# Performance work log

Hardware: AMD Instinct MI355X
Metric: run time of the kernel (lower is better)

## Reference

```python
import jax, jax.numpy as jnp
import numpy as np

N = 2048
E = 512
H = 8
DH = E // H
L = 2
MAX_DIST = 10
LOCAL_DIST = 2
NUM_COLORS = 16
NEG_INF = -1e9


def _layer_norm(x, scale, bias, eps=1e-5):
    mu = jnp.mean(x, axis=-1, keepdims=True)
    var = jnp.mean(jnp.square(x - mu), axis=-1, keepdims=True)
    return (x - mu) * jax.lax.rsqrt(var + eps) * scale + bias


def setup_inputs() -> dict:
    key = jax.random.key(0)
    ks = jax.random.split(key, 12)
    s = 0.05  # weight init scale for numerical sanity
    return {
        "D": jax.random.randint(ks[0], (N, N), 0, MAX_DIST + 2, dtype=jnp.int32),
        "x": jax.random.normal(ks[1], (1, N, E), dtype=jnp.float32),
        "dist_emb": jax.random.normal(ks[2], (MAX_DIST + 2, 8), dtype=jnp.float32) * s,
        "dist_proj_w": jax.random.normal(ks[3], (1, 8), dtype=jnp.float32) * s,
        "dist_proj_b": jnp.zeros((1,), jnp.float32),
        "ln1_scale": jnp.ones((L, E), jnp.float32),
        "ln1_bias": jnp.zeros((L, E), jnp.float32),
        "in_proj_w": jax.random.normal(ks[4], (L, 3 * E, E), dtype=jnp.float32) * s,
        "in_proj_b": jnp.zeros((L, 3 * E), jnp.float32),
        "out_w": jax.random.normal(ks[5], (L, E, E), dtype=jnp.float32) * s,
        "out_b": jnp.zeros((L, E), jnp.float32),
        "ln2_scale": jnp.ones((L, E), jnp.float32),
        "ln2_bias": jnp.zeros((L, E), jnp.float32),
        "ff1_w": jax.random.normal(ks[6], (L, 2 * E, E), dtype=jnp.float32) * s,
        "ff1_b": jnp.zeros((L, 2 * E), jnp.float32),
        "ff2_w": jax.random.normal(ks[7], (L, E, 2 * E), dtype=jnp.float32) * s,
        "ff2_b": jnp.zeros((L, E), jnp.float32),
        "color_w": jax.random.normal(ks[8], (NUM_COLORS, E), dtype=jnp.float32) * s,
        "color_b": jnp.zeros((NUM_COLORS,), jnp.float32),
    }


def reference(D, x, dist_emb, dist_proj_w, dist_proj_b,
              ln1_scale, ln1_bias, in_proj_w, in_proj_b, out_w, out_b,
              ln2_scale, ln2_bias, ff1_w, ff1_b, ff2_w, ff2_b,
              color_w, color_b):
    # Distance encoder: clamp -> embed -> project to scalar bias per (i, j)
    d_clamped = jnp.clip(D, 0, MAX_DIST + 1)                        # [N, N]
    emb = dist_emb[d_clamped]                                       # [N, N, 8]
    bias = jnp.einsum('nme,e->nm', emb, dist_proj_w[0]) + dist_proj_b[0]
    # Graph-local sparsity: real bias within local_dist, -inf elsewhere
    attn_mask = jnp.where(D <= LOCAL_DIST, bias, NEG_INF)           # [N, N]

    scale = 1.0 / jnp.sqrt(jnp.asarray(DH, x.dtype))
    for l in range(L):
        # --- pre-norm multihead self-attention ---
        xn = _layer_norm(x, ln1_scale[l], ln1_bias[l])              # [1, N, E]
        qkv = jnp.einsum('bne,fe->bnf', xn, in_proj_w[l]) + in_proj_b[l]
        q, k, v = jnp.split(qkv, 3, axis=-1)                        # each [1, N, E]
        q = q.reshape(1, N, H, DH)
        k = k.reshape(1, N, H, DH)
        v = v.reshape(1, N, H, DH)
        scores = jnp.einsum('bnhd,bmhd->bhnm', q, k) * scale        # [1, H, N, N]
        scores = scores + attn_mask[None, None, :, :]
        probs = jax.nn.softmax(scores, axis=-1)
        attn = jnp.einsum('bhnm,bmhd->bnhd', probs, v).reshape(1, N, E)
        attn = jnp.einsum('bne,fe->bnf', attn, out_w[l]) + out_b[l]
        x = x + attn                                                # dropout = identity (eval)
        # --- pre-norm feed-forward ---
        xf = _layer_norm(x, ln2_scale[l], ln2_bias[l])
        h = jax.nn.relu(jnp.einsum('bne,fe->bnf', xf, ff1_w[l]) + ff1_b[l])
        ff = jnp.einsum('bnf,ef->bne', h, ff2_w[l]) + ff2_b[l]
        x = x + ff

    logits = jnp.einsum('bne,ce->bnc', x, color_w) + color_b        # [1, N, C]
    return jax.nn.softmax(logits, axis=-1)[0]                       # [N, C]
```

## Files before the change

### kernel.cpp

```cpp
#include <hip/hip_runtime.h>
#include <cstddef>
#include <cstdint>

#define NN 2048
#define EE 512
#define HH 8
#define QKVF 1536
#define NSEG 4

typedef __attribute__((ext_vector_type(4))) float f32x4;
typedef __attribute__((ext_vector_type(8))) short s16x8;
typedef __attribute__((ext_vector_type(4))) short s16x4;

static __device__ __forceinline__ unsigned short f2bf(float x) {
  union { float f; unsigned int u; } c; c.f = x;
  unsigned int r = (c.u + 0x7FFFu + ((c.u >> 16) & 1u)) >> 16;
  return (unsigned short)r;
}
static __device__ __forceinline__ float bf2f(unsigned short b) {
  union { unsigned int u; float f; } c; c.u = ((unsigned int)b) << 16;
  return c.f;
}

#define GLL16(gp, lp) __builtin_amdgcn_global_load_lds( \
    (const __attribute__((address_space(1))) void*)(gp), \
    (__attribute__((address_space(3))) void*)(lp), 16, 0, 0)

__global__ __launch_bounds__(256) void cvt_all(
    const float* __restrict__ s0, const float* __restrict__ s1,
    const float* __restrict__ s2, const float* __restrict__ s3,
    unsigned short* __restrict__ d0, unsigned short* __restrict__ d1,
    unsigned short* __restrict__ d2, unsigned short* __restrict__ d3,
    int n0, int n1, int n2, int n3) {
  int j = blockIdx.x * 256 + threadIdx.x;
  const float* s; unsigned short* d;
  if (j < n0) { s = s0; d = d0; }
  else {
    j -= n0;
    if (j < n1) { s = s1; d = d1; }
    else {
      j -= n1;
      if (j < n2) { s = s2; d = d2; }
      else { j -= n2; if (j >= n3) return; s = s3; d = d3; }
    }
  }
  float4 v = ((const float4*)s)[j];
  s16x4 o;
  o[0] = (short)f2bf(v.x); o[1] = (short)f2bf(v.y);
  o[2] = (short)f2bf(v.z); o[3] = (short)f2bf(v.w);
  ((s16x4*)d)[j] = o;
}

__global__ __launch_bounds__(256) void mask_pack(const int* __restrict__ D,
    unsigned int* __restrict__ codes) {
  int id = blockIdx.x * 256 + threadIdx.x;
  int row = id >> 9;
  int u = id & 511;
  int ch = u >> 4, col = u & 15;
  int base = ch * 64 + col;
  unsigned int pk = 0;
#pragma unroll
  for (int i = 0; i < 4; i++) {
    int d = D[(size_t)row * NN + base + 16 * i];
    unsigned int c = (d <= 2) ? (unsigned int)d : 3u;
    pk |= c << (8 * i);
  }
  codes[id] = pk;
}

__global__ __launch_bounds__(256) void ln_kernel(const float* __restrict__ x,
    const float* __restrict__ scale, const float* __restrict__ bias,
    unsigned short* __restrict__ out) {
  int row = blockIdx.x;
  int t = threadIdx.x;
  const float* xr = x + (size_t)row * EE;
  float a = xr[t], b = xr[t + 256];
  float s = a + b, q = a * a + b * b;
#pragma unroll
  for (int m = 1; m < 64; m <<= 1) {
    s += __shfl_xor(s, m);
    q += __shfl_xor(q, m);
  }
  __shared__ float ps[4], pq[4];
  int w = t >> 6;
  if ((t & 63) == 0) { ps[w] = s; pq[w] = q; }
  __syncthreads();
  s = ps[0] + ps[1] + ps[2] + ps[3];
  q = pq[0] + pq[1] + pq[2] + pq[3];
  float mu = s * (1.f / EE);
  float var = q * (1.f / EE) - mu * mu;
  float r = rsqrtf(var + 1e-5f);
  unsigned short* orow = out + (size_t)row * EE;
  orow[t] = f2bf((a - mu) * r * scale[t] + bias[t]);
  orow[t + 256] = f2bf((b - mu) * r * scale[t + 256] + bias[t + 256]);
}

template <int RELU, int RES, int OBF>
__global__ __launch_bounds__(256) void gemm_bf(
    const unsigned short* __restrict__ A, const unsigned short* __restrict__ B,
    const float* __restrict__ bias, const float* __restrict__ R,
    void* __restrict__ Cout, int M, int F, int K) {
  __shared__ __attribute__((aligned(16))) unsigned short Al[2][64 * 64];
  __shared__ __attribute__((aligned(16))) unsigned short Bl[2][64 * 64];
  const int t = threadIdx.x;
  const int w = t >> 6, l = t & 63;
  const int fr = l & 15, fs = l >> 4;
  const int bm = blockIdx.y * 64, bf = blockIdx.x * 64;
  const int srow = l >> 3, slot = l & 7;
  const int nk = K >> 6;

  f32x4 acc[4];
  f32x4 zero = {0.f, 0.f, 0.f, 0.f};
#pragma unroll
  for (int j = 0; j < 4; j++) acc[j] = zero;

  auto stage = [&](int kt, int bsel) {
    int k0 = kt * 64;
#pragma unroll
    for (int rnd = 0; rnd < 2; rnd++) {
      int rowblk = w * 2 + rnd;
      int row = rowblk * 8 + srow;
      int koff = (slot * 8) ^ ((row & 7) * 8);
      GLL16(A + (size_t)(bm + row) * K + k0 + koff, &Al[bsel][rowblk * 512]);
      GLL16(B + (size_t)(bf + row) * K + k0 + koff, &Bl[bsel][rowblk * 512]);
    }
  };

  stage(0, 0);
  __syncthreads();
  for (int kt = 0; kt < nk; kt++) {
    const int cur = kt & 1;
    if (kt + 1 < nk) stage(kt + 1, cur ^ 1);
    s16x8 af[2], bg[4][2];
    const int arow = w * 16 + fr;
#pragma unroll
    for (int ks = 0; ks < 2; ks++)
      af[ks] = *(const s16x8*)&Al[cur][arow * 64 + ((ks * 32 + fs * 8) ^ ((arow & 7) * 8))];
#pragma unroll
    for (int ni = 0; ni < 4; ni++)
#pragma unroll
      for (int ks = 0; ks < 2; ks++) {
        int row = 16 * ni + fr;
        bg[ni][ks] = *(const s16x8*)&Bl[cur][row * 64 + ((ks * 32 + fs * 8) ^ ((row & 7) * 8))];
      }
#pragma unroll
    for (int ni = 0; ni < 4; ni++)
#pragma unroll
      for (int ks = 0; ks < 2; ks++)
        acc[ni] = __builtin_amdgcn_mfma_f32_16x16x32_bf16(af[ks], bg[ni][ks], acc[ni], 0, 0, 0);
    __syncthreads();
  }

#pragma unroll
  for (int ni = 0; ni < 4; ni++) {
    int gcol = bf + 16 * ni + fr;
    float bb = bias[gcol];
#pragma unroll
    for (int r = 0; r < 4; r++) {
      int grow = bm + w * 16 + fs * 4 + r;
      float v = acc[ni][r] + bb;
      if (RELU) v = fmaxf(v, 0.f);
      if (RES) v += R[(size_t)grow * F + gcol];
      if (OBF) ((unsigned short*)Cout)[(size_t)grow * F + gcol] = f2bf(v);
      else ((float*)Cout)[(size_t)grow * F + gcol] = v;
    }
  }
}

__global__ __launch_bounds__(256) void attn_mfma(
    const unsigned short* __restrict__ qkv, const unsigned int* __restrict__ codes,
    const float* __restrict__ demb, const float* __restrict__ dpw,
    const float* __restrict__ dpb, float* __restrict__ po, float* __restrict__ lpart) {
  __shared__ __attribute__((aligned(16))) unsigned short Kl[64 * 64];
  __shared__ __attribute__((aligned(16))) unsigned short Vt[64 * 64];
  __shared__ __attribute__((aligned(16))) unsigned short Pl[4][16 * 64];
  const int t = threadIdx.x;
  const int w = t >> 6, l = t & 63;
  const int fr = l & 15, fs = l >> 4;
  const int h = blockIdx.y;
  const int seg = blockIdx.z;
  const int qrow0 = blockIdx.x * 64 + w * 16;
  const int kvbase = seg * (NN / NSEG);
  const float C2 = 0.18033688011112042f;

  float w0, w1, w2;
  {
    float s0 = 0.f, s1 = 0.f, s2 = 0.f;
#pragma unroll
    for (int e = 0; e < 8; e++) {
      float pw = dpw[e];
      s0 += demb[e] * pw; s1 += demb[8 + e] * pw; s2 += demb[16 + e] * pw;
    }
    float b = dpb[0];
    w0 = __expf(s0 + b); w1 = __expf(s1 + b); w2 = __expf(s2 + b);
  }

  s16x8 qf[2];
#pragma unroll
  for (int ks = 0; ks < 2; ks++)
    qf[ks] = *(const s16x8*)&qkv[(size_t)(qrow0 + fr) * QKVF + h * 64 + ks * 32 + fs * 8];

  f32x4 o[4];
  float lacc[4];
  f32x4 zero = {0.f, 0.f, 0.f, 0.f};
#pragma unroll
  for (int i = 0; i < 4; i++) { o[i] = zero; lacc[i] = 0.f; }

  const int krow = t >> 2, kc = (t & 3) * 16;
  const int vkv = (t & 15) * 4, vd = (t >> 4) * 4;
  const unsigned short* kbase = qkv + EE + h * 64;
  const unsigned short* vbase = qkv + 2 * EE + h * 64;
  s16x8 kreg[2];
  s16x4 vreg[4];
#pragma unroll
  for (int i = 0; i < 2; i++)
    kreg[i] = *(const s16x8*)&kbase[(size_t)(kvbase + krow) * QKVF + kc + i * 8];
#pragma unroll
  for (int i = 0; i < 4; i++)
    vreg[i] = *(const s16x4*)&vbase[(size_t)(kvbase + vkv + i) * QKVF + vd];

  for (int ch = 0; ch < NN / NSEG / 64; ch++) {
    __syncthreads();
#pragma unroll
    for (int i = 0; i < 2; i++)
      *(s16x8*)&Kl[krow * 64 + ((kc + i * 8) ^ ((krow & 7) * 8))] = kreg[i];
#pragma unroll
    for (int dj = 0; dj < 4; dj++) {
      int d = vd + dj;
      s16x4 pk;
      pk[0] = vreg[0][dj]; pk[1] = vreg[1][dj]; pk[2] = vreg[2][dj]; pk[3] = vreg[3][dj];
      *(s16x4*)&Vt[d * 64 + (vkv ^ ((d & 7) * 8))] = pk;
    }
    __syncthreads();
    if (ch + 1 < NN / NSEG / 64) {
      int kv0 = kvbase + (ch + 1) * 64;
#pragma unroll
      for (int i = 0; i < 2; i++)
        kreg[i] = *(const s16x8*)&kbase[(size_t)(kv0 + krow) * QKVF + kc + i * 8];
#pragma unroll
      for (int i = 0; i < 4; i++)
        vreg[i] = *(const s16x4*)&vbase[(size_t)(kv0 + vkv + i) * QKVF + vd];
    }
    int gc = kvbase / 64 + ch;
    unsigned int cd[4];
#pragma unroll
    for (int r = 0; r < 4; r++)
      cd[r] = codes[(size_t)(qrow0 + fs * 4 + r) * (NN / 4) + gc * 16 + fr];

    f32x4 s[4];
#pragma unroll
    for (int ni = 0; ni < 4; ni++) s[ni] = zero;
    __builtin_amdgcn_s_setprio(1);
#pragma unroll
    for (int ni = 0; ni < 4; ni++) {
      int row = 16 * ni + fr;
#pragma unroll
      for (int ks = 0; ks < 2; ks++) {
        s16x8 kf = *(const s16x8*)&Kl[row * 64 + ((ks * 32 + fs * 8) ^ ((row & 7) * 8))];
        s[ni] = __builtin_amdgcn_mfma_f32_16x16x32_bf16(qf[ks], kf, s[ni], 0, 0, 0);
      }
    }
    __builtin_amdgcn_s_setprio(0);
#pragma unroll
    for (int r = 0; r < 4; r++) {
      int prow = fs * 4 + r;
      float psum = 0.f;
#pragma unroll
      for (int ni = 0; ni < 4; ni++) {
        unsigned int code = (cd[r] >> (8 * ni)) & 255u;
        float wsel = code == 0u ? w0 : (code == 1u ? w1 : (code == 2u ? w2 : 0.f));
        float p = exp2f(s[ni][r] * C2) * wsel;
        unsigned short pb = f2bf(p);
        psum += bf2f(pb);
        Pl[w][prow * 64 + ((16 * ni + fr) ^ ((prow & 7) * 8))] = pb;
      }
      lacc[r] += psum;
    }
    __builtin_amdgcn_s_setprio(1);
#pragma unroll
    for (int ks = 0; ks < 2; ks++) {
      s16x8 pa = *(const s16x8*)&Pl[w][fr * 64 + ((ks * 32 + fs * 8) ^ ((fr & 7) * 8))];
#pragma unroll
      for (int dn = 0; dn < 4; dn++) {
        int row = 16 * dn + fr;
        s16x8 vf = *(const s16x8*)&Vt[row * 64 + ((ks * 32 + fs * 8) ^ ((row & 7) * 8))];
        o[dn] = __builtin_amdgcn_mfma_f32_16x16x32_bf16(pa, vf, o[dn], 0, 0, 0);
      }
    }
    __builtin_amdgcn_s_setprio(0);
  }
#pragma unroll
  for (int r = 0; r < 4; r++) {
#pragma unroll
    for (int m = 1; m < 16; m <<= 1) lacc[r] += __shfl_xor(lacc[r], m);
  }
#pragma unroll
  for (int r = 0; r < 4; r++) {
    int row = qrow0 + fs * 4 + r;
#pragma unroll
    for (int dn = 0; dn < 4; dn++)
      po[((size_t)seg * NN + row) * EE + h * 64 + 16 * dn + fr] = o[dn][r];
    if (fr == 0) lpart[((size_t)seg * NN + row) * 8 + h] = lacc[r];
  }
}

__global__ __launch_bounds__(256) void attn_combine(const float* __restrict__ po,
    const float* __restrict__ lpart, unsigned short* __restrict__ attnb) {
  int id = blockIdx.x * 256 + threadIdx.x;
  int row = id >> 7;
  int col = (id & 127) * 4;
  int h = col >> 6;
  float4 o = {0.f, 0.f, 0.f, 0.f};
  float lsum = 0.f;
#pragma unroll
  for (int s = 0; s < NSEG; s++) {
    float4 p4 = *(const float4*)&po[((size_t)s * NN + row) * EE + col];
    o.x += p4.x; o.y += p4.y; o.z += p4.z; o.w += p4.w;
    lsum += lpart[((size_t)s * NN + row) * 8 + h];
  }
  float inv = 1.f / lsum;
  s16x4 ob;
  ob[0] = (short)f2bf(o.x * inv); ob[1] = (short)f2bf(o.y * inv);
  ob[2] = (short)f2bf(o.z * inv); ob[3] = (short)f2bf(o.w * inv);
  *(s16x4*)&attnb[(size_t)row * EE + col] = ob;
}

__global__ __launch_bounds__(256) void logits_kernel(const float* __restrict__ x,
    const float* __restrict__ cw, const float* __restrict__ cb,
    float* __restrict__ out) {
  int t = threadIdx.x;
  int wv = t >> 6, lane = t & 63;
  int row = blockIdx.x * 4 + wv;
  const float* xr = x + (size_t)row * EE;
  int c = lane >> 2, p = lane & 3;
  const float* w = cw + c * EE;
  float s = 0.f;
  for (int e = p * 128; e < p * 128 + 128; e++) s += xr[e] * w[e];
  s += __shfl_xor(s, 1);
  s += __shfl_xor(s, 2);
  __shared__ float lg[4][16];
  if (p == 0) lg[wv][c] = s + cb[c];
  __syncthreads();
  if (lane < 16) {
    float mx = -INFINITY;
#pragma unroll
    for (int k = 0; k < 16; k++) mx = fmaxf(mx, lg[wv][k]);
    float sum = 0.f;
#pragma unroll
    for (int k = 0; k < 16; k++) sum += __expf(lg[wv][k] - mx);
    out[(size_t)row * 16 + lane] = __expf(lg[wv][lane] - mx) / sum;
  }
}

extern "C" void kernel_launch(void* const* d_in, const int* in_sizes, int n_in,
                              void* d_out, int out_size, void* d_ws, size_t ws_size,
                              hipStream_t stream) {
  const int* D = (const int*)d_in[0];
  const float* x = (const float*)d_in[1];
  const float* demb = (const float*)d_in[2];
  const float* dpw = (const float*)d_in[3];
  const float* dpb = (const float*)d_in[4];
  const float* ln1s = (const float*)d_in[5];
  const float* ln1b = (const float*)d_in[6];
  const float* ipw = (const float*)d_in[7];
  const float* ipb = (const float*)d_in[8];
  const float* ow = (const float*)d_in[9];
  const float* ob = (const float*)d_in[10];
  const float* ln2s = (const float*)d_in[11];
  const float* ln2b = (const float*)d_in[12];
  const float* f1w = (const float*)d_in[13];
  const float* f1b = (const float*)d_in[14];
  const float* f2w = (const float*)d_in[15];
  const float* f2b = (const float*)d_in[16];
  const float* cw = (const float*)d_in[17];
  const float* cb = (const float*)d_in[18];

  char* base = (char*)d_ws;
  unsigned int* codes = (unsigned int*)base;
  float* xbuf = (float*)(base + (4u << 20));
  unsigned short* qkv = (unsigned short*)(base + (8u << 20));
  unsigned short* xn = (unsigned short*)(base + (14u << 20));
  unsigned short* attnb = (unsigned short*)(base + (16u << 20));
  unsigned short* hbuf = (unsigned short*)(base + (18u << 20));
  unsigned short* ipw_bf = (unsigned short*)(base + (22u << 20));
  unsigned short* ow_bf = (unsigned short*)(base + (25u << 20));
  unsigned short* f1w_bf = (unsigned short*)(base + (26u << 20));
  unsigned short* f2w_bf = (unsigned short*)(base + (28u << 20));
  float* po = (float*)(base + (31u << 20));
  float* lpart = (float*)(base + (47u << 20));

  cvt_all<<<4096, 256, 0, stream>>>(ipw, ow, f1w, f2w,
      ipw_bf, ow_bf, f1w_bf, f2w_bf, 393216, 131072, 262144, 262144);
  mask_pack<<<4096, 256, 0, stream>>>(D, codes);

  for (int l = 0; l < 2; l++) {
    const float* xin = (l == 0) ? x : xbuf;
    ln_kernel<<<NN, 256, 0, stream>>>(xin, ln1s + l * EE, ln1b + l * EE, xn);
    gemm_bf<0, 0, 1><<<dim3(24, 32), 256, 0, stream>>>(
        xn, ipw_bf + (size_t)l * 786432, ipb + l * 1536, nullptr, qkv, NN, 1536, 512);
    attn_mfma<<<dim3(32, HH, NSEG), 256, 0, stream>>>(qkv, codes, demb, dpw, dpb, po, lpart);
    attn_combine<<<1024, 256, 0, stream>>>(po, lpart, attnb);
    gemm_bf<0, 1, 0><<<dim3(8, 32), 256, 0, stream>>>(
        attnb, ow_bf + (size_t)l * 262144, ob + l * EE, xin, xbuf, NN, 512, 512);
    ln_kernel<<<NN, 256, 0, stream>>>(xbuf, ln2s + l * EE, ln2b + l * EE, xn);
    gemm_bf<1, 0, 1><<<dim3(16, 32), 256, 0, stream>>>(
        xn, f1w_bf + (size_t)l * 524288, f1b + l * 1024, nullptr, hbuf, NN, 1024, 512);
    gemm_bf<0, 1, 0><<<dim3(8, 32), 256, 0, stream>>>(
        hbuf, f2w_bf + (size_t)l * 524288, f2b + l * EE, xbuf, xbuf, NN, 512, 1024);
  }
  logits_kernel<<<NN / 4, 256, 0, stream>>>(xbuf, cw, cb, (float*)d_out);
}
```

Before: 316.0 us.

## Precompute per-pair mask weights, fold row-sum into MFMA, double KV split

Merges the weight conversion and mask packing into one prep kernel that stores the exponentiated distance weights as fp32 per (row, key) pair, so the attention loop no longer decodes codes. The softmax row sum is now produced by an extra MFMA against a row of ones in the V tile instead of scalar accumulation plus shuffles. Probabilities are truncated to bf16 rather than rounded. The key/value split count doubles from 4 to 8 to raise parallelism. In exchange, the mask array is four times larger (16MB instead of 4MB) and the partial-output buffers and combine pass also double in size.

```diff
diff --git a/kernel.cpp b/kernel.cpp
--- a/kernel.cpp
+++ b/kernel.cpp
@@ -6,7 +6,7 @@
 #define EE 512
 #define HH 8
 #define QKVF 1536
-#define NSEG 4
+#define NSEG 8
 
 typedef __attribute__((ext_vector_type(4))) float f32x4;
 typedef __attribute__((ext_vector_type(8))) short s16x8;
@@ -17,55 +17,59 @@
   unsigned int r = (c.u + 0x7FFFu + ((c.u >> 16) & 1u)) >> 16;
   return (unsigned short)r;
 }
-static __device__ __forceinline__ float bf2f(unsigned short b) {
-  union { unsigned int u; float f; } c; c.u = ((unsigned int)b) << 16;
-  return c.f;
-}
 
 #define GLL16(gp, lp) __builtin_amdgcn_global_load_lds( \
     (const __attribute__((address_space(1))) void*)(gp), \
     (__attribute__((address_space(3))) void*)(lp), 16, 0, 0)
 
-__global__ __launch_bounds__(256) void cvt_all(
+__global__ __launch_bounds__(256) void prep(
     const float* __restrict__ s0, const float* __restrict__ s1,
     const float* __restrict__ s2, const float* __restrict__ s3,
     unsigned short* __restrict__ d0, unsigned short* __restrict__ d1,
     unsigned short* __restrict__ d2, unsigned short* __restrict__ d3,
-    int n0, int n1, int n2, int n3) {
-  int j = blockIdx.x * 256 + threadIdx.x;
-  const float* s; unsigned short* d;
-  if (j < n0) { s = s0; d = d0; }
-  else {
-    j -= n0;
-    if (j < n1) { s = s1; d = d1; }
+    const int* __restrict__ D, const float* __restrict__ demb,
+    const float* __restrict__ dpw, const float* __restrict__ dpb,
+    float* __restrict__ wpk4) {
+  int b = blockIdx.x;
+  if (b < 4096) {
+    int j = b * 256 + threadIdx.x;
+    const float* s; unsigned short* d;
+    if (j < 393216) { s = s0; d = d0; }
     else {
-      j -= n1;
-      if (j < n2) { s = s2; d = d2; }
-      else { j -= n2; if (j >= n3) return; s = s3; d = d3; }
-    }
-  }
-  float4 v = ((const float4*)s)[j];
-  s16x4 o;
-  o[0] = (short)f2bf(v.x); o[1] = (short)f2bf(v.y);
-  o[2] = (short)f2bf(v.z); o[3] = (short)f2bf(v.w);
-  ((s16x4*)d)[j] = o;
-}
-
-__global__ __launch_bounds__(256) void mask_pack(const int* __restrict__ D,
-    unsigned int* __restrict__ codes) {
-  int id = blockIdx.x * 256 + threadIdx.x;
-  int row = id >> 9;
-  int u = id & 511;
-  int ch = u >> 4, col = u & 15;
-  int base = ch * 64 + col;
-  unsigned int pk = 0;
-#pragma unroll
-  for (int i = 0; i < 4; i++) {
-    int d = D[(size_t)row * NN + base + 16 * i];
-    unsigned int c = (d <= 2) ? (unsigned int)d : 3u;
-    pk |= c << (8 * i);
-  }
-  codes[id] = pk;
+      j -= 393216;
+      if (j < 131072) { s = s1; d = d1; }
+      else {
+        j -= 131072;
+        if (j < 262144) { s = s2; d = d2; }
+        else { j -= 262144; s = s3; d = d3; }
+      }
+    }
+    float4 v = ((const float4*)s)[j];
+    s16x4 o;
+    o[0] = (short)f2bf(v.x); o[1] = (short)f2bf(v.y);
+    o[2] = (short)f2bf(v.z); o[3] = (short)f2bf(v.w);
+    ((s16x4*)d)[j] = o;
+  } else {
+    int e = (b - 4096) * 256 + threadIdx.x;
+    float ws0 = 0.f, ws1 = 0.f, ws2 = 0.f;
+#pragma unroll
+    for (int k = 0; k < 8; k++) {
+      float pw = dpw[k];
+      ws0 += demb[k] * pw; ws1 += demb[8 + k] * pw; ws2 += demb[16 + k] * pw;
+    }
+    float bb = dpb[0];
+    float w0 = __expf(ws0 + bb), w1 = __expf(ws1 + bb), w2 = __expf(ws2 + bb);
+    int row = e >> 9;
+    int u = e & 511;
+    int base = (u >> 4) * 64 + (u & 15);
+    f32x4 wv;
+#pragma unroll
+    for (int i = 0; i < 4; i++) {
+      int d = D[(size_t)row * NN + base + 16 * i];
+      wv[i] = (d == 0) ? w0 : (d == 1) ? w1 : (d == 2) ? w2 : 0.f;
+    }
+    ((f32x4*)wpk4)[e] = wv;
+  }
 }
 
 __global__ __launch_bounds__(256) void ln_kernel(const float* __restrict__ x,
@@ -168,11 +172,10 @@
 }
 
 __global__ __launch_bounds__(256) void attn_mfma(
-    const unsigned short* __restrict__ qkv, const unsigned int* __restrict__ codes,
-    const float* __restrict__ demb, const float* __restrict__ dpw,
-    const float* __restrict__ dpb, float* __restrict__ po, float* __restrict__ lpart) {
+    const unsigned short* __restrict__ qkv, const float* __restrict__ wpk4,
+    float* __restrict__ po, float* __restrict__ lpart) {
   __shared__ __attribute__((aligned(16))) unsigned short Kl[64 * 64];
-  __shared__ __attribute__((aligned(16))) unsigned short Vt[64 * 64];
+  __shared__ __attribute__((aligned(16))) unsigned short Vt[66 * 64];
   __shared__ __attribute__((aligned(16))) unsigned short Pl[4][16 * 64];
   const int t = threadIdx.x;
   const int w = t >> 6, l = t & 63;
@@ -183,28 +186,18 @@
   const int kvbase = seg * (NN / NSEG);
   const float C2 = 0.18033688011112042f;
 
-  float w0, w1, w2;
-  {
-    float s0 = 0.f, s1 = 0.f, s2 = 0.f;
-#pragma unroll
-    for (int e = 0; e < 8; e++) {
-      float pw = dpw[e];
-      s0 += demb[e] * pw; s1 += demb[8 + e] * pw; s2 += demb[16 + e] * pw;
-    }
-    float b = dpb[0];
-    w0 = __expf(s0 + b); w1 = __expf(s1 + b); w2 = __expf(s2 + b);
-  }
+  if (t < 64) Vt[64 * 64 + t] = 0x3F80;
 
   s16x8 qf[2];
 #pragma unroll
   for (int ks = 0; ks < 2; ks++)
     qf[ks] = *(const s16x8*)&qkv[(size_t)(qrow0 + fr) * QKVF + h * 64 + ks * 32 + fs * 8];
 
-  f32x4 o[4];
-  float lacc[4];
+  f32x4 o[4], o4;
   f32x4 zero = {0.f, 0.f, 0.f, 0.f};
 #pragma unroll
-  for (int i = 0; i < 4; i++) { o[i] = zero; lacc[i] = 0.f; }
+  for (int i = 0; i < 4; i++) o[i] = zero;
+  o4 = zero;
 
   const int krow = t >> 2, kc = (t & 3) * 16;
   const int vkv = (t & 15) * 4, vd = (t >> 4) * 4;
@@ -242,10 +235,6 @@
         vreg[i] = *(const s16x4*)&vbase[(size_t)(kv0 + vkv + i) * QKVF + vd];
     }
     int gc = kvbase / 64 + ch;
-    unsigned int cd[4];
-#pragma unroll
-    for (int r = 0; r < 4; r++)
-      cd[r] = codes[(size_t)(qrow0 + fs * 4 + r) * (NN / 4) + gc * 16 + fr];
 
     f32x4 s[4];
 #pragma unroll
@@ -264,17 +253,14 @@
 #pragma unroll
     for (int r = 0; r < 4; r++) {
       int prow = fs * 4 + r;
-      float psum = 0.f;
+      f32x4 wv = *(const f32x4*)&wpk4[((size_t)(qrow0 + prow) * 512 + gc * 16 + fr) * 4];
 #pragma unroll
       for (int ni = 0; ni < 4; ni++) {
-        unsigned int code = (cd[r] >> (8 * ni)) & 255u;
-        float wsel = code == 0u ? w0 : (code == 1u ? w1 : (code == 2u ? w2 : 0.f));
-        float p = exp2f(s[ni][r] * C2) * wsel;
-        unsigned short pb = f2bf(p);
-        psum += bf2f(pb);
-        Pl[w][prow * 64 + ((16 * ni + fr) ^ ((prow & 7) * 8))] = pb;
-      }
-      lacc[r] += psum;
+        union { float f; unsigned int u; } c;
+        c.f = exp2f(s[ni][r] * C2) * wv[ni];
+        Pl[w][prow * 64 + ((16 * ni + fr) ^ ((prow & 7) * 8))] =
+            (unsigned short)(c.u >> 16);
+      }
     }
     __builtin_amdgcn_s_setprio(1);
 #pragma unroll
@@ -286,13 +272,10 @@
         s16x8 vf = *(const s16x8*)&Vt[row * 64 + ((ks * 32 + fs * 8) ^ ((row & 7) * 8))];
         o[dn] = __builtin_amdgcn_mfma_f32_16x16x32_bf16(pa, vf, o[dn], 0, 0, 0);
       }
+      s16x8 vf4 = *(const s16x8*)&Vt[(64 + fr) * 64 + ((ks * 32 + fs * 8) ^ ((fr & 7) * 8))];
+      o4 = __builtin_amdgcn_mfma_f32_16x16x32_bf16(pa, vf4, o4, 0, 0, 0);
     }
     __builtin_amdgcn_s_setprio(0);
-  }
-#pragma unroll
-  for (int r = 0; r < 4; r++) {
-#pragma unroll
-    for (int m = 1; m < 16; m <<= 1) lacc[r] += __shfl_xor(lacc[r], m);
   }
 #pragma unroll
   for (int r = 0; r < 4; r++) {
@@ -300,7 +283,7 @@
 #pragma unroll
     for (int dn = 0; dn < 4; dn++)
       po[((size_t)seg * NN + row) * EE + h * 64 + 16 * dn + fr] = o[dn][r];
-    if (fr == 0) lpart[((size_t)seg * NN + row) * 8 + h] = lacc[r];
+    if (fr == 0) lpart[((size_t)seg * NN + row) * 8 + h] = o4[r];
   }
 }
 
@@ -376,29 +359,28 @@
   const float* cb = (const float*)d_in[18];
 
   char* base = (char*)d_ws;
-  unsigned int* codes = (unsigned int*)base;
-  float* xbuf = (float*)(base + (4u << 20));
-  unsigned short* qkv = (unsigned short*)(base + (8u << 20));
-  unsigned short* xn = (unsigned short*)(base + (14u << 20));
-  unsigned short* attnb = (unsigned short*)(base + (16u << 20));
-  unsigned short* hbuf = (unsigned short*)(base + (18u << 20));
-  unsigned short* ipw_bf = (unsigned short*)(base + (22u << 20));
-  unsigned short* ow_bf = (unsigned short*)(base + (25u << 20));
-  unsigned short* f1w_bf = (unsigned short*)(base + (26u << 20));
-  unsigned short* f2w_bf = (unsigned short*)(base + (28u << 20));
-  float* po = (float*)(base + (31u << 20));
-  float* lpart = (float*)(base + (47u << 20));
-
-  cvt_all<<<4096, 256, 0, stream>>>(ipw, ow, f1w, f2w,
-      ipw_bf, ow_bf, f1w_bf, f2w_bf, 393216, 131072, 262144, 262144);
-  mask_pack<<<4096, 256, 0, stream>>>(D, codes);
+  float* wpk4 = (float*)base;
+  float* xbuf = (float*)(base + (16u << 20));
+  unsigned short* qkv = (unsigned short*)(base + (20u << 20));
+  unsigned short* xn = (unsigned short*)(base + (26u << 20));
+  unsigned short* attnb = (unsigned short*)(base + (28u << 20));
+  unsigned short* hbuf = (unsigned short*)(base + (30u << 20));
+  unsigned short* ipw_bf = (unsigned short*)(base + (34u << 20));
+  unsigned short* ow_bf = (unsigned short*)(base + (37u << 20));
+  unsigned short* f1w_bf = (unsigned short*)(base + (38u << 20));
+  unsigned short* f2w_bf = (unsigned short*)(base + (40u << 20));
+  float* po = (float*)(base + (42u << 20));
+  float* lpart = (float*)(base + (74u << 20));
+
+  prep<<<8192, 256, 0, stream>>>(ipw, ow, f1w, f2w,
+      ipw_bf, ow_bf, f1w_bf, f2w_bf, D, demb, dpw, dpb, wpk4);
 
   for (int l = 0; l < 2; l++) {
     const float* xin = (l == 0) ? x : xbuf;
     ln_kernel<<<NN, 256, 0, stream>>>(xin, ln1s + l * EE, ln1b + l * EE, xn);
     gemm_bf<0, 0, 1><<<dim3(24, 32), 256, 0, stream>>>(
         xn, ipw_bf + (size_t)l * 786432, ipb + l * 1536, nullptr, qkv, NN, 1536, 512);
-    attn_mfma<<<dim3(32, HH, NSEG), 256, 0, stream>>>(qkv, codes, demb, dpw, dpb, po, lpart);
+    attn_mfma<<<dim3(32, HH, NSEG), 256, 0, stream>>>(qkv, wpk4, po, lpart);
     attn_combine<<<1024, 256, 0, stream>>>(po, lpart, attnb);
     gemm_bf<0, 1, 0><<<dim3(8, 32), 256, 0, stream>>>(
         attnb, ow_bf + (size_t)l * 262144, ob + l * EE, xin, xbuf, NN, 512, 512);
```

Measured after the change: 300.3 us. 1.05x faster.
